# Performance work log

Measured on AMD Instinct MI355X. Metric: run time of the kernel, lower is better.

## Reference

```python
import jax, jax.numpy as jnp
import numpy as np

B, S, D_IN = 4, 2048, 1024
H, D_HEAD = 16, 64  # per-head output dim d_output=64


def setup_inputs() -> dict:
    key = jax.random.key(0)
    ks = jax.random.split(key, 9)
    s_in = 1.0 / np.sqrt(D_IN)
    s_o = 1.0 / np.sqrt(H * D_HEAD)
    return {
        "x": jax.random.normal(ks[0], (B, S, D_IN), dtype=jnp.float32),
        "Wq": jax.random.uniform(ks[1], (H, D_IN, D_HEAD), jnp.float32, -s_in, s_in),
        "bq": jax.random.uniform(ks[2], (H, D_HEAD), jnp.float32, -s_in, s_in),
        "Wk": jax.random.uniform(ks[3], (H, D_IN, D_HEAD), jnp.float32, -s_in, s_in),
        "bk": jax.random.uniform(ks[4], (H, D_HEAD), jnp.float32, -s_in, s_in),
        "Wv": jax.random.uniform(ks[5], (H, D_IN, D_HEAD), jnp.float32, -s_in, s_in),
        "bv": jax.random.uniform(ks[6], (H, D_HEAD), jnp.float32, -s_in, s_in),
        "Wo": jax.random.uniform(ks[7], (H * D_HEAD, D_HEAD), jnp.float32, -s_o, s_o),
        "bo": jax.random.uniform(ks[8], (D_HEAD,), jnp.float32, -s_o, s_o),
    }


def reference(x, Wq, bq, Wk, bk, Wv, bv, Wo, bo):
    # per-head projections: [B,H,S,Dh]
    q = jnp.einsum("bsd,hde->bhse", x, Wq) + bq[None, :, None, :]
    k = jnp.einsum("bsd,hde->bhse", x, Wk) + bk[None, :, None, :]
    v = jnp.einsum("bsd,hde->bhse", x, Wv) + bv[None, :, None, :]
    scale = 1.0 / np.sqrt(D_HEAD)
    scores = jnp.einsum("bhqe,bhke->bhqk", q, k) * scale  # [B,H,S,S]
    seq_len = x.shape[1]
    causal = jnp.tril(jnp.ones((seq_len, seq_len), dtype=bool))
    scores = jnp.where(causal[None, None], scores, -jnp.inf)
    attn = jax.nn.softmax(scores, axis=-1)  # dropout=0 -> identity
    out = jnp.einsum("bhqk,bhke->bhqe", attn, v)  # [B,H,S,Dh]
    # concat heads along feature dim (head order matches torch cat)
    out = out.transpose(0, 2, 1, 3).reshape(x.shape[0], seq_len, H * D_HEAD)
    return out @ Wo + bo
```

## Files before the change

kernel.cpp:

```cpp
#include <hip/hip_runtime.h>

typedef unsigned short u16;
typedef unsigned int u32;
typedef __attribute__((ext_vector_type(8))) short s16x8;
typedef __attribute__((ext_vector_type(4))) float f32x4;

#define MFMA(a,b,c) __builtin_amdgcn_mfma_f32_16x16x32_bf16((a),(b),(c),0,0,0)
#define QSCALE 0.18033688011112042f

__device__ __forceinline__ u16 bfc(float f){
  union { float f; unsigned int u; } c; c.f = f;
  return (u16)((c.u + 0x7fffu + ((c.u >> 16) & 1u)) >> 16);
}
__device__ __forceinline__ u32 pkbf(float lo, float hi){
  union { float f; u32 u; } a, b; a.f = lo; b.f = hi;
  return __builtin_amdgcn_perm(b.u + 0x8000u, a.u + 0x8000u, 0x07060302u);
}
__device__ __forceinline__ float fexp2(float x){ return __builtin_amdgcn_exp2f(x); }
__device__ __forceinline__ f32x4 zero4(){ f32x4 z; z[0]=0.f; z[1]=0.f; z[2]=0.f; z[3]=0.f; return z; }

__device__ __forceinline__ void gload_lds16(const u16* g, u16* l){
  __builtin_amdgcn_global_load_lds((const __attribute__((address_space(1))) unsigned int*)g,
                                   (__attribute__((address_space(3))) unsigned int*)l, 16, 0, 0);
}

__global__ __launch_bounds__(256) void k_cvt(const float* __restrict__ x, u16* __restrict__ xb){
  int i = (blockIdx.x * 256 + threadIdx.x) * 4;
  float4 v = *(const float4*)(x + i);
  *(uint2*)(xb + i) = make_uint2(pkbf(v.x, v.y), pkbf(v.z, v.w));
}

__global__ __launch_bounds__(256) void k_twp(const float* __restrict__ Wq, const float* __restrict__ Wk,
    const float* __restrict__ Wv, const float* __restrict__ Wo,
    u16* __restrict__ wt, u16* __restrict__ wot){
  __shared__ float t[64][65];
  int y = blockIdx.y, k0 = blockIdx.x * 64, tid = threadIdx.x;
  const float* src; u16* dst;
  if (y < 16)      { src = Wq + (size_t)y * 65536;        dst = wt + (size_t)y * 65536; }
  else if (y < 32) { src = Wk + (size_t)(y-16) * 65536;   dst = wt + (size_t)y * 65536; }
  else if (y < 48) { src = Wv + (size_t)(y-32) * 65536;   dst = wt + (size_t)y * 65536; }
  else             { src = Wo;                            dst = wot; }
  const float* s = src + (size_t)k0 * 64;
  int kl = tid >> 2, nc = (tid & 3) * 16;
  #pragma unroll
  for (int j = 0; j < 4; j++){
    float4 v = *(const float4*)(s + kl * 64 + nc + j * 4);
    t[kl][nc + j*4 + 0] = v.x; t[kl][nc + j*4 + 1] = v.y;
    t[kl][nc + j*4 + 2] = v.z; t[kl][nc + j*4 + 3] = v.w;
  }
  __syncthreads();
  int n = tid >> 2, kc = (tid & 3) * 16;
  u16 o[16];
  #pragma unroll
  for (int j = 0; j < 16; j++) o[j] = bfc(t[kc + j][n]);
  u16* d = dst + (size_t)n * 1024 + k0 + kc;
  *(uint4*)(d)     = *(uint4*)&o[0];
  *(uint4*)(d + 8) = *(uint4*)&o[8];
}

__global__ __launch_bounds__(256) void k_qkv(const u16* __restrict__ xb, const u16* __restrict__ wt,
    const float* __restrict__ bq, const float* __restrict__ bk, const float* __restrict__ bv,
    u16* __restrict__ Qo, u16* __restrict__ Ko, u16* __restrict__ VT){
  __shared__ u16 As[128][64];
  __shared__ u16 Bs[128][64];
  int tid = threadIdx.x, wave = tid >> 6, lane = tid & 63;
  int l16 = lane & 15, g = lane >> 4;
  int row0 = blockIdx.x * 128, col0 = blockIdx.y * 128;
  int wm = (wave & 1) * 64, wn = (wave >> 1) * 64;
  f32x4 acc[4][4];
  #pragma unroll
  for (int mt = 0; mt < 4; mt++)
    #pragma unroll
    for (int nt = 0; nt < 4; nt++) acc[mt][nt] = zero4();
  int srow = (lane >> 3);
  int scol = ((lane & 7) ^ srow) * 8;
  for (int k0 = 0; k0 < 1024; k0 += 64){
    __syncthreads();
    #pragma unroll
    for (int p = 0; p < 4; p++){
      int r = wave * 32 + p * 8 + srow;
      gload_lds16(xb + (size_t)(row0 + r) * 1024 + k0 + scol, &As[wave * 32 + p * 8][0]);
      gload_lds16(wt + (size_t)(col0 + r) * 1024 + k0 + scol, &Bs[wave * 32 + p * 8][0]);
    }
    __syncthreads();
    #pragma unroll
    for (int c = 0; c < 2; c++){
      s16x8 af[4], bf[4];
      #pragma unroll
      for (int mt = 0; mt < 4; mt++)
        af[mt] = *(const s16x8*)&As[wm + mt*16 + l16][((c*4 + g) ^ (l16 & 7)) * 8];
      #pragma unroll
      for (int nt = 0; nt < 4; nt++)
        bf[nt] = *(const s16x8*)&Bs[wn + nt*16 + l16][((c*4 + g) ^ (l16 & 7)) * 8];
      #pragma unroll
      for (int mt = 0; mt < 4; mt++)
        #pragma unroll
        for (int nt = 0; nt < 4; nt++) acc[mt][nt] = MFMA(af[mt], bf[nt], acc[mt][nt]);
    }
  }
  #pragma unroll
  for (int nt = 0; nt < 4; nt++){
    int n = col0 + wn + nt * 16 + l16;
    int wi = n >> 10, hh = (n >> 6) & 15, dh = n & 63;
    const float* bptr = (wi == 0) ? bq : (wi == 1) ? bk : bv;
    float bval = bptr[hh * 64 + dh];
    #pragma unroll
    for (int mt = 0; mt < 4; mt++){
      int m0 = row0 + wm + mt * 16 + g * 4;
      int bb = m0 >> 11, ss = m0 & 2047;
      if (wi == 2){
        u32 p0 = pkbf(acc[mt][nt][0] + bval, acc[mt][nt][1] + bval);
        u32 p1 = pkbf(acc[mt][nt][2] + bval, acc[mt][nt][3] + bval);
        *(uint2*)&VT[(((size_t)bb * 16 + hh) * 64 + dh) * 2048 + ss] = make_uint2(p0, p1);
      } else {
        u16* dst = (wi == 0) ? Qo : Ko;
        float scl = (wi == 0) ? QSCALE : 1.0f;
        #pragma unroll
        for (int i = 0; i < 4; i++)
          dst[(((size_t)bb * 16 + hh) * 2048 + ss + i) * 64 + dh] = bfc((acc[mt][nt][i] + bval) * scl);
      }
    }
  }
}

__global__ __launch_bounds__(256, 2) void k_attn(const u16* __restrict__ Q, const u16* __restrict__ Kg,
    const u16* __restrict__ VT, u16* __restrict__ O){
  __shared__ u16 smem[18432];
  u16* Ks = smem;
  u16* Vt = smem + 4608;
  u16* Ps = smem + 9216;
  float* mg = (float*)smem;
  float* lg = (float*)smem + 8192;
  int hbi = blockIdx.x, pair = blockIdx.y;
  int b = hbi >> 4, h = hbi & 15;
  int tid = threadIdx.x, wave = tid >> 6, lane = tid & 63;
  int l16 = lane & 15, g = lane >> 4;
  int qg = wave >> 1, kg = wave & 1;
  size_t hb = (size_t)hbi * 2048 * 64;
  const u16* kbase = Kg + hb;
  const u16* vbase = VT + hb;
  int sr = tid >> 3, scc = (tid & 7) * 8;
  u16* PsW = Ps + wave * (4 * 16 * 36);
  #pragma unroll
  for (int ph = 0; ph < 2; ph++){
    int qt = ph ? pair : (15 - pair);
    int qbase = qt * 128;
    int q0 = qbase + qg * 64;
    s16x8 bq[4][2];
    #pragma unroll
    for (int j = 0; j < 4; j++)
      #pragma unroll
      for (int c = 0; c < 2; c++)
        bq[j][c] = *(const s16x8*)(Q + hb + (size_t)(q0 + j*16 + l16) * 64 + c*32 + g*8);
    f32x4 accO[4][4];
    #pragma unroll
    for (int mt = 0; mt < 4; mt++)
      #pragma unroll
      for (int j = 0; j < 4; j++) accO[mt][j] = zero4();
    f32x4 rsacc = zero4();
    int nkt = 2 * qt + 2;
    uint4 ka0, ka1, va0, va1;
    __syncthreads();
    ka0 = *(const uint4*)(kbase + (size_t)(sr)      * 64 + scc);
    ka1 = *(const uint4*)(kbase + (size_t)(sr + 32) * 64 + scc);
    va0 = *(const uint4*)(vbase + (size_t)(sr)      * 2048 + scc);
    va1 = *(const uint4*)(vbase + (size_t)(sr + 32) * 2048 + scc);
    *(uint4*)&Ks[sr * 72 + scc] = ka0; *(uint4*)&Ks[(sr + 32) * 72 + scc] = ka1;
    *(uint4*)&Vt[sr * 72 + scc] = va0; *(uint4*)&Vt[(sr + 32) * 72 + scc] = va1;
    __syncthreads();
    for (int kt = 0; kt < nkt; kt++){
      if (kt + 1 < nkt){
        int kb2 = (kt + 1) * 64;
        ka0 = *(const uint4*)(kbase + (size_t)(kb2 + sr)      * 64 + scc);
        ka1 = *(const uint4*)(kbase + (size_t)(kb2 + sr + 32) * 64 + scc);
        va0 = *(const uint4*)(vbase + (size_t)(sr)      * 2048 + kb2 + scc);
        va1 = *(const uint4*)(vbase + (size_t)(sr + 32) * 2048 + kb2 + scc);
      }
      int ks0 = kt * 64 + kg * 32;
      if (ks0 <= q0 + 63){
        s16x8 ak[2][2], av[4];
        #pragma unroll
        for (int t = 0; t < 2; t++)
          #pragma unroll
          for (int c = 0; c < 2; c++)
            ak[t][c] = *(const s16x8*)&Ks[(kg*32 + t*16 + l16) * 72 + c*32 + g*8];
        #pragma unroll
        for (int mt = 0; mt < 4; mt++)
          av[mt] = *(const s16x8*)&Vt[(mt*16 + l16) * 72 + kg*32 + g*8];
        #pragma unroll
        for (int j = 0; j < 4; j++){
          f32x4 s0 = zero4(), s1 = zero4();
          s0 = MFMA(ak[0][0], bq[j][0], s0);
          s0 = MFMA(ak[0][1], bq[j][1], s0);
          s1 = MFMA(ak[1][0], bq[j][0], s1);
          s1 = MFMA(ak[1][1], bq[j][1], s1);
          if (ks0 + 31 > q0 + j*16){
            int qrow = q0 + j*16 + l16;
            #pragma unroll
            for (int r = 0; r < 4; r++){
              if (ks0 + g*4 + r      > qrow) s0[r] = -1e30f;
              if (ks0 + 16 + g*4 + r > qrow) s1[r] = -1e30f;
            }
          }
          float p00 = fexp2(s0[0]), p01 = fexp2(s0[1]), p02 = fexp2(s0[2]), p03 = fexp2(s0[3]);
          float p10 = fexp2(s1[0]), p11 = fexp2(s1[1]), p12 = fexp2(s1[2]), p13 = fexp2(s1[3]);
          rsacc[j] += ((p00 + p01) + (p02 + p03)) + ((p10 + p11) + (p12 + p13));
          u16* pr = PsW + (j*16 + l16) * 36;
          *(uint2*)&pr[g*4]      = make_uint2(pkbf(p00, p01), pkbf(p02, p03));
          *(uint2*)&pr[16 + g*4] = make_uint2(pkbf(p10, p11), pkbf(p12, p13));
        }
        #pragma unroll
        for (int j = 0; j < 4; j++){
          s16x8 bp = *(const s16x8*)&PsW[(j*16 + l16) * 36 + g*8];
          #pragma unroll
          for (int mt = 0; mt < 4; mt++)
            accO[mt][j] = MFMA(av[mt], bp, accO[mt][j]);
        }
      }
      if (kt + 1 < nkt){
        __syncthreads();
        *(uint4*)&Ks[sr * 72 + scc] = ka0; *(uint4*)&Ks[(sr + 32) * 72 + scc] = ka1;
        *(uint4*)&Vt[sr * 72 + scc] = va0; *(uint4*)&Vt[(sr + 32) * 72 + scc] = va1;
        __syncthreads();
      }
    }
    __syncthreads();
    if (kg == 1){
      #pragma unroll
      for (int mt = 0; mt < 4; mt++)
        #pragma unroll
        for (int j = 0; j < 4; j++)
          *(f32x4*)&mg[((qg*16 + mt*4 + j) * 64 + lane) * 4] = accO[mt][j];
      *(f32x4*)&lg[(qg*64 + lane) * 4] = rsacc;
    }
    __syncthreads();
    if (kg == 0){
      f32x4 lpart = *(f32x4*)&lg[(qg*64 + lane) * 4];
      float rinv[4];
      #pragma unroll
      for (int j = 0; j < 4; j++){
        float l = rsacc[j] + lpart[j];
        l += __shfl_xor(l, 16);
        l += __shfl_xor(l, 32);
        rinv[j] = 1.0f / l;
      }
      #pragma unroll
      for (int mt = 0; mt < 4; mt++)
        #pragma unroll
        for (int j = 0; j < 4; j++){
          f32x4 part = *(f32x4*)&mg[((qg*16 + mt*4 + j) * 64 + lane) * 4];
          float o0 = (accO[mt][j][0] + part[0]) * rinv[j];
          float o1 = (accO[mt][j][1] + part[1]) * rinv[j];
          float o2 = (accO[mt][j][2] + part[2]) * rinv[j];
          float o3 = (accO[mt][j][3] + part[3]) * rinv[j];
          *(uint2*)&O[((size_t)b * 2048 + q0 + j*16 + l16) * 1024 + h*64 + mt*16 + g*4] =
              make_uint2(pkbf(o0, o1), pkbf(o2, o3));
        }
    }
  }
}

__global__ __launch_bounds__(256) void k_oproj(const u16* __restrict__ Ob, const u16* __restrict__ wot,
    const float* __restrict__ bo, float* __restrict__ out){
  __shared__ u16 As[64][72];
  __shared__ u16 Bs[64][72];
  int rb = blockIdx.x, kc = blockIdx.y;
  int tid = threadIdx.x, wave = tid >> 6, lane = tid & 63;
  int l16 = lane & 15, g = lane >> 4;
  int wr = (wave & 1) * 32, wc = (wave >> 1) * 32;
  int row0 = rb * 64;
  f32x4 acc[2][2];
  acc[0][0]=zero4(); acc[0][1]=zero4(); acc[1][0]=zero4(); acc[1][1]=zero4();
  int r0s = tid >> 3, cc0 = (tid & 7) * 8, r1s = r0s + 32;
  for (int k0 = kc * 256; k0 < kc * 256 + 256; k0 += 64){
    __syncthreads();
    *(uint4*)&As[r0s][cc0] = *(const uint4*)(Ob + (size_t)(row0 + r0s) * 1024 + k0 + cc0);
    *(uint4*)&As[r1s][cc0] = *(const uint4*)(Ob + (size_t)(row0 + r1s) * 1024 + k0 + cc0);
    *(uint4*)&Bs[r0s][cc0] = *(const uint4*)(wot + (size_t)r0s * 1024 + k0 + cc0);
    *(uint4*)&Bs[r1s][cc0] = *(const uint4*)(wot + (size_t)r1s * 1024 + k0 + cc0);
    __syncthreads();
    #pragma unroll
    for (int c = 0; c < 2; c++){
      int kcc = c * 32;
      s16x8 a0 = *(const s16x8*)&As[wr      + l16][kcc + g * 8];
      s16x8 a1 = *(const s16x8*)&As[wr + 16 + l16][kcc + g * 8];
      s16x8 b0 = *(const s16x8*)&Bs[wc      + l16][kcc + g * 8];
      s16x8 b1 = *(const s16x8*)&Bs[wc + 16 + l16][kcc + g * 8];
      acc[0][0] = MFMA(a0, b0, acc[0][0]);
      acc[0][1] = MFMA(a0, b1, acc[0][1]);
      acc[1][0] = MFMA(a1, b0, acc[1][0]);
      acc[1][1] = MFMA(a1, b1, acc[1][1]);
    }
  }
  #pragma unroll
  for (int rt = 0; rt < 2; rt++){
    #pragma unroll
    for (int ct = 0; ct < 2; ct++){
      int col = wc + ct * 16 + l16;
      float bval = (kc == 0) ? bo[col] : 0.f;
      #pragma unroll
      for (int i = 0; i < 4; i++){
        int row = row0 + wr + rt * 16 + g * 4 + i;
        atomicAdd(&out[(size_t)row * 64 + col], acc[rt][ct][i] + bval);
      }
    }
  }
}

extern "C" void kernel_launch(void* const* d_in, const int* in_sizes, int n_in,
                              void* d_out, int out_size, void* d_ws, size_t ws_size,
                              hipStream_t stream){
  const float* x  = (const float*)d_in[0];
  const float* Wq = (const float*)d_in[1];
  const float* bq = (const float*)d_in[2];
  const float* Wk = (const float*)d_in[3];
  const float* bk = (const float*)d_in[4];
  const float* Wv = (const float*)d_in[5];
  const float* bv = (const float*)d_in[6];
  const float* Wo = (const float*)d_in[7];
  const float* bo = (const float*)d_in[8];

  u16* xb  = (u16*)d_ws;
  u16* wt  = xb  + 8388608;
  u16* wot = wt  + 3145728;
  u16* Qb  = wot + 65536;
  u16* Kb  = Qb  + 8388608;
  u16* VTb = Kb  + 8388608;
  u16* Ob  = xb;
  float* out = (float*)d_out;

  hipMemsetAsync(d_out, 0, (size_t)out_size * sizeof(float), stream);
  k_cvt<<<8192, 256, 0, stream>>>(x, xb);
  k_twp<<<dim3(16, 49), 256, 0, stream>>>(Wq, Wk, Wv, Wo, wt, wot);
  k_qkv<<<dim3(64, 24), 256, 0, stream>>>(xb, wt, bq, bk, bv, Qb, Kb, VTb);
  k_attn<<<dim3(64, 8), 256, 0, stream>>>(Qb, Kb, VTb, Ob);
  k_oproj<<<dim3(128, 4), 256, 0, stream>>>(Ob, wot, bo, out);
}
```

Before: 244.9 us.

## Drop shared K/V staging in attention and split work across 8 waves

The attention kernel stops staging K and V tiles through shared memory with block-wide barriers. Each wave now loads its K and V fragments straight from global memory (relying on cache) and skips fully masked tiles independently. The block grows to 512 threads, with each wave owning 32 query rows instead of 64, which halves per-wave accumulators and should raise occupancy. The trade-off is that K/V data is read redundantly by several waves from global/L2 instead of being shared in LDS.

Measured after the change: 299.5 us. 1.22x slower.

```diff
diff --git a/kernel.cpp b/kernel.cpp
--- a/kernel.cpp
+++ b/kernel.cpp
@@ -123,12 +123,9 @@
   }
 }
 
-__global__ __launch_bounds__(256, 2) void k_attn(const u16* __restrict__ Q, const u16* __restrict__ Kg,
+__global__ __launch_bounds__(512, 4) void k_attn(const u16* __restrict__ Q, const u16* __restrict__ Kg,
     const u16* __restrict__ VT, u16* __restrict__ O){
-  __shared__ u16 smem[18432];
-  u16* Ks = smem;
-  u16* Vt = smem + 4608;
-  u16* Ps = smem + 9216;
+  __shared__ u16 smem[17408];
   float* mg = (float*)smem;
   float* lg = (float*)smem + 8192;
   int hbi = blockIdx.x, pair = blockIdx.y;
@@ -139,89 +136,67 @@
   size_t hb = (size_t)hbi * 2048 * 64;
   const u16* kbase = Kg + hb;
   const u16* vbase = VT + hb;
-  int sr = tid >> 3, scc = (tid & 7) * 8;
-  u16* PsW = Ps + wave * (4 * 16 * 36);
+  u16* PsW = smem + wave * 1152;
+  const u16* vrow[4];
+  #pragma unroll
+  for (int mt = 0; mt < 4; mt++) vrow[mt] = vbase + (size_t)(mt*16 + l16) * 2048 + g*8;
   #pragma unroll
   for (int ph = 0; ph < 2; ph++){
     int qt = ph ? pair : (15 - pair);
     int qbase = qt * 128;
-    int q0 = qbase + qg * 64;
-    s16x8 bq[4][2];
-    #pragma unroll
-    for (int j = 0; j < 4; j++)
+    int q0 = qbase + qg * 32;
+    s16x8 bq[2][2];
+    #pragma unroll
+    for (int j = 0; j < 2; j++)
       #pragma unroll
       for (int c = 0; c < 2; c++)
         bq[j][c] = *(const s16x8*)(Q + hb + (size_t)(q0 + j*16 + l16) * 64 + c*32 + g*8);
-    f32x4 accO[4][4];
-    #pragma unroll
-    for (int mt = 0; mt < 4; mt++)
-      #pragma unroll
-      for (int j = 0; j < 4; j++) accO[mt][j] = zero4();
-    f32x4 rsacc = zero4();
+    f32x4 accO[4][2];
+    #pragma unroll
+    for (int mt = 0; mt < 4; mt++){ accO[mt][0] = zero4(); accO[mt][1] = zero4(); }
+    float rsacc[2] = {0.f, 0.f};
     int nkt = 2 * qt + 2;
-    uint4 ka0, ka1, va0, va1;
-    __syncthreads();
-    ka0 = *(const uint4*)(kbase + (size_t)(sr)      * 64 + scc);
-    ka1 = *(const uint4*)(kbase + (size_t)(sr + 32) * 64 + scc);
-    va0 = *(const uint4*)(vbase + (size_t)(sr)      * 2048 + scc);
-    va1 = *(const uint4*)(vbase + (size_t)(sr + 32) * 2048 + scc);
-    *(uint4*)&Ks[sr * 72 + scc] = ka0; *(uint4*)&Ks[(sr + 32) * 72 + scc] = ka1;
-    *(uint4*)&Vt[sr * 72 + scc] = va0; *(uint4*)&Vt[(sr + 32) * 72 + scc] = va1;
     __syncthreads();
     for (int kt = 0; kt < nkt; kt++){
-      if (kt + 1 < nkt){
-        int kb2 = (kt + 1) * 64;
-        ka0 = *(const uint4*)(kbase + (size_t)(kb2 + sr)      * 64 + scc);
-        ka1 = *(const uint4*)(kbase + (size_t)(kb2 + sr + 32) * 64 + scc);
-        va0 = *(const uint4*)(vbase + (size_t)(sr)      * 2048 + kb2 + scc);
-        va1 = *(const uint4*)(vbase + (size_t)(sr + 32) * 2048 + kb2 + scc);
-      }
       int ks0 = kt * 64 + kg * 32;
-      if (ks0 <= q0 + 63){
-        s16x8 ak[2][2], av[4];
-        #pragma unroll
-        for (int t = 0; t < 2; t++)
+      if (ks0 > q0 + 31) continue;
+      s16x8 ak[2][2], av[4];
+      #pragma unroll
+      for (int t = 0; t < 2; t++)
+        #pragma unroll
+        for (int c = 0; c < 2; c++)
+          ak[t][c] = *(const s16x8*)(kbase + (size_t)(ks0 + t*16 + l16) * 64 + c*32 + g*8);
+      #pragma unroll
+      for (int mt = 0; mt < 4; mt++)
+        av[mt] = *(const s16x8*)(vrow[mt] + ks0);
+      #pragma unroll
+      for (int j = 0; j < 2; j++){
+        f32x4 s0 = zero4(), s1 = zero4();
+        s0 = MFMA(ak[0][0], bq[j][0], s0);
+        s0 = MFMA(ak[0][1], bq[j][1], s0);
+        s1 = MFMA(ak[1][0], bq[j][0], s1);
+        s1 = MFMA(ak[1][1], bq[j][1], s1);
+        if (ks0 + 31 > q0 + j*16){
+          int qrow = q0 + j*16 + l16;
           #pragma unroll
-          for (int c = 0; c < 2; c++)
-            ak[t][c] = *(const s16x8*)&Ks[(kg*32 + t*16 + l16) * 72 + c*32 + g*8];
+          for (int r = 0; r < 4; r++){
+            if (ks0 + g*4 + r      > qrow) s0[r] = -1e30f;
+            if (ks0 + 16 + g*4 + r > qrow) s1[r] = -1e30f;
+          }
+        }
+        float p00 = fexp2(s0[0]), p01 = fexp2(s0[1]), p02 = fexp2(s0[2]), p03 = fexp2(s0[3]);
+        float p10 = fexp2(s1[0]), p11 = fexp2(s1[1]), p12 = fexp2(s1[2]), p13 = fexp2(s1[3]);
+        rsacc[j] += ((p00 + p01) + (p02 + p03)) + ((p10 + p11) + (p12 + p13));
+        u16* pr = PsW + (j*16 + l16) * 36;
+        *(uint2*)&pr[g*4]      = make_uint2(pkbf(p00, p01), pkbf(p02, p03));
+        *(uint2*)&pr[16 + g*4] = make_uint2(pkbf(p10, p11), pkbf(p12, p13));
+      }
+      #pragma unroll
+      for (int j = 0; j < 2; j++){
+        s16x8 bp = *(const s16x8*)&PsW[(j*16 + l16) * 36 + g*8];
         #pragma unroll
         for (int mt = 0; mt < 4; mt++)
-          av[mt] = *(const s16x8*)&Vt[(mt*16 + l16) * 72 + kg*32 + g*8];
-        #pragma unroll
-        for (int j = 0; j < 4; j++){
-          f32x4 s0 = zero4(), s1 = zero4();
-          s0 = MFMA(ak[0][0], bq[j][0], s0);
-          s0 = MFMA(ak[0][1], bq[j][1], s0);
-          s1 = MFMA(ak[1][0], bq[j][0], s1);
-          s1 = MFMA(ak[1][1], bq[j][1], s1);
-          if (ks0 + 31 > q0 + j*16){
-            int qrow = q0 + j*16 + l16;
-            #pragma unroll
-            for (int r = 0; r < 4; r++){
-              if (ks0 + g*4 + r      > qrow) s0[r] = -1e30f;
-              if (ks0 + 16 + g*4 + r > qrow) s1[r] = -1e30f;
-            }
-          }
-          float p00 = fexp2(s0[0]), p01 = fexp2(s0[1]), p02 = fexp2(s0[2]), p03 = fexp2(s0[3]);
-          float p10 = fexp2(s1[0]), p11 = fexp2(s1[1]), p12 = fexp2(s1[2]), p13 = fexp2(s1[3]);
-          rsacc[j] += ((p00 + p01) + (p02 + p03)) + ((p10 + p11) + (p12 + p13));
-          u16* pr = PsW + (j*16 + l16) * 36;
-          *(uint2*)&pr[g*4]      = make_uint2(pkbf(p00, p01), pkbf(p02, p03));
-          *(uint2*)&pr[16 + g*4] = make_uint2(pkbf(p10, p11), pkbf(p12, p13));
-        }
-        #pragma unroll
-        for (int j = 0; j < 4; j++){
-          s16x8 bp = *(const s16x8*)&PsW[(j*16 + l16) * 36 + g*8];
-          #pragma unroll
-          for (int mt = 0; mt < 4; mt++)
-            accO[mt][j] = MFMA(av[mt], bp, accO[mt][j]);
-        }
-      }
-      if (kt + 1 < nkt){
-        __syncthreads();
-        *(uint4*)&Ks[sr * 72 + scc] = ka0; *(uint4*)&Ks[(sr + 32) * 72 + scc] = ka1;
-        *(uint4*)&Vt[sr * 72 + scc] = va0; *(uint4*)&Vt[(sr + 32) * 72 + scc] = va1;
-        __syncthreads();
+          accO[mt][j] = MFMA(av[mt], bp, accO[mt][j]);
       }
     }
     __syncthreads();
@@ -229,17 +204,17 @@
       #pragma unroll
       for (int mt = 0; mt < 4; mt++)
         #pragma unroll
-        for (int j = 0; j < 4; j++)
-          *(f32x4*)&mg[((qg*16 + mt*4 + j) * 64 + lane) * 4] = accO[mt][j];
-      *(f32x4*)&lg[(qg*64 + lane) * 4] = rsacc;
+        for (int j = 0; j < 2; j++)
+          *(f32x4*)&mg[((qg*8 + mt*2 + j) * 64 + lane) * 4] = accO[mt][j];
+      lg[(qg*64 + lane)*2 + 0] = rsacc[0];
+      lg[(qg*64 + lane)*2 + 1] = rsacc[1];
     }
     __syncthreads();
     if (kg == 0){
-      f32x4 lpart = *(f32x4*)&lg[(qg*64 + lane) * 4];
-      float rinv[4];
-      #pragma unroll
-      for (int j = 0; j < 4; j++){
-        float l = rsacc[j] + lpart[j];
+      float rinv[2];
+      #pragma unroll
+      for (int j = 0; j < 2; j++){
+        float l = rsacc[j] + lg[(qg*64 + lane)*2 + j];
         l += __shfl_xor(l, 16);
         l += __shfl_xor(l, 32);
         rinv[j] = 1.0f / l;
@@ -247,8 +222,8 @@
       #pragma unroll
       for (int mt = 0; mt < 4; mt++)
         #pragma unroll
-        for (int j = 0; j < 4; j++){
-          f32x4 part = *(f32x4*)&mg[((qg*16 + mt*4 + j) * 64 + lane) * 4];
+        for (int j = 0; j < 2; j++){
+          f32x4 part = *(f32x4*)&mg[((qg*8 + mt*2 + j) * 64 + lane) * 4];
           float o0 = (accO[mt][j][0] + part[0]) * rinv[j];
           float o1 = (accO[mt][j][1] + part[1]) * rinv[j];
           float o2 = (accO[mt][j][2] + part[2]) * rinv[j];
@@ -333,6 +308,6 @@
   k_cvt<<<8192, 256, 0, stream>>>(x, xb);
   k_twp<<<dim3(16, 49), 256, 0, stream>>>(Wq, Wk, Wv, Wo, wt, wot);
   k_qkv<<<dim3(64, 24), 256, 0, stream>>>(xb, wt, bq, bk, bv, Qb, Kb, VTb);
-  k_attn<<<dim3(64, 8), 256, 0, stream>>>(Qb, Kb, VTb, Ob);
+  k_attn<<<dim3(64, 8), 512, 0, stream>>>(Qb, Kb, VTb, Ob);
   k_oproj<<<dim3(128, 4), 256, 0, stream>>>(Ob, wot, bo, out);
 }
```

## Merge conversion kernels and stage 128-key K/V tiles per barrier in attention

Applied to the files above, without the earlier changes.

Merges the x conversion and weight transpose kernels into one launch, with a flat block index deciding which job each block does. The attention kernel now loads 128 keys of K and V per stage instead of 64 and processes them as two 64-key substeps. This halves the number of barrier pairs and global-to-LDS staging rounds. The cost is more LDS (about 54KB) and more staging registers, which may limit occupancy at two blocks per CU.

Result: slower. 292.0 us (+19.2%).

```diff
diff --git a/kernel.cpp b/kernel.cpp
--- a/kernel.cpp
+++ b/kernel.cpp
@@ -24,17 +24,20 @@
                                    (__attribute__((address_space(3))) unsigned int*)l, 16, 0, 0);
 }
 
-__global__ __launch_bounds__(256) void k_cvt(const float* __restrict__ x, u16* __restrict__ xb){
-  int i = (blockIdx.x * 256 + threadIdx.x) * 4;
-  float4 v = *(const float4*)(x + i);
-  *(uint2*)(xb + i) = make_uint2(pkbf(v.x, v.y), pkbf(v.z, v.w));
-}
-
-__global__ __launch_bounds__(256) void k_twp(const float* __restrict__ Wq, const float* __restrict__ Wk,
+__global__ __launch_bounds__(256) void k_prep(const float* __restrict__ x, u16* __restrict__ xb,
+    const float* __restrict__ Wq, const float* __restrict__ Wk,
     const float* __restrict__ Wv, const float* __restrict__ Wo,
     u16* __restrict__ wt, u16* __restrict__ wot){
   __shared__ float t[64][65];
-  int y = blockIdx.y, k0 = blockIdx.x * 64, tid = threadIdx.x;
+  int bid = blockIdx.x, tid = threadIdx.x;
+  if (bid < 8192){
+    int i = (bid * 256 + tid) * 4;
+    float4 v = *(const float4*)(x + i);
+    *(uint2*)(xb + i) = make_uint2(pkbf(v.x, v.y), pkbf(v.z, v.w));
+    return;
+  }
+  int tt = bid - 8192;
+  int y = tt >> 4, k0 = (tt & 15) * 64;
   const float* src; u16* dst;
   if (y < 16)      { src = Wq + (size_t)y * 65536;        dst = wt + (size_t)y * 65536; }
   else if (y < 32) { src = Wk + (size_t)(y-16) * 65536;   dst = wt + (size_t)y * 65536; }
@@ -125,10 +128,10 @@
 
 __global__ __launch_bounds__(256, 2) void k_attn(const u16* __restrict__ Q, const u16* __restrict__ Kg,
     const u16* __restrict__ VT, u16* __restrict__ O){
-  __shared__ u16 smem[18432];
+  __shared__ u16 smem[27136];
   u16* Ks = smem;
-  u16* Vt = smem + 4608;
-  u16* Ps = smem + 9216;
+  u16* Vt = smem + 9216;
+  u16* Ps = smem + 17920;
   float* mg = (float*)smem;
   float* lg = (float*)smem + 8192;
   int hbi = blockIdx.x, pair = blockIdx.y;
@@ -140,7 +143,8 @@
   const u16* kbase = Kg + hb;
   const u16* vbase = VT + hb;
   int sr = tid >> 3, scc = (tid & 7) * 8;
-  u16* PsW = Ps + wave * (4 * 16 * 36);
+  int vr = tid >> 4, vcc = (tid & 15) * 8;
+  u16* PsW = Ps + wave * 2304;
   #pragma unroll
   for (int ph = 0; ph < 2; ph++){
     int qt = ph ? pair : (15 - pair);
@@ -158,69 +162,81 @@
       #pragma unroll
       for (int j = 0; j < 4; j++) accO[mt][j] = zero4();
     f32x4 rsacc = zero4();
-    int nkt = 2 * qt + 2;
-    uint4 ka0, ka1, va0, va1;
-    __syncthreads();
-    ka0 = *(const uint4*)(kbase + (size_t)(sr)      * 64 + scc);
-    ka1 = *(const uint4*)(kbase + (size_t)(sr + 32) * 64 + scc);
-    va0 = *(const uint4*)(vbase + (size_t)(sr)      * 2048 + scc);
-    va1 = *(const uint4*)(vbase + (size_t)(sr + 32) * 2048 + scc);
-    *(uint4*)&Ks[sr * 72 + scc] = ka0; *(uint4*)&Ks[(sr + 32) * 72 + scc] = ka1;
-    *(uint4*)&Vt[sr * 72 + scc] = va0; *(uint4*)&Vt[(sr + 32) * 72 + scc] = va1;
-    __syncthreads();
-    for (int kt = 0; kt < nkt; kt++){
-      if (kt + 1 < nkt){
-        int kb2 = (kt + 1) * 64;
-        ka0 = *(const uint4*)(kbase + (size_t)(kb2 + sr)      * 64 + scc);
-        ka1 = *(const uint4*)(kbase + (size_t)(kb2 + sr + 32) * 64 + scc);
-        va0 = *(const uint4*)(vbase + (size_t)(sr)      * 2048 + kb2 + scc);
-        va1 = *(const uint4*)(vbase + (size_t)(sr + 32) * 2048 + kb2 + scc);
-      }
-      int ks0 = kt * 64 + kg * 32;
-      if (ks0 <= q0 + 63){
-        s16x8 ak[2][2], av[4];
-        #pragma unroll
-        for (int t = 0; t < 2; t++)
+    int nst = qt + 1;
+    uint4 ka[4], va[4];
+    __syncthreads();
+    #pragma unroll
+    for (int m = 0; m < 4; m++){
+      ka[m] = *(const uint4*)(kbase + (size_t)(sr + 32*m) * 64 + scc);
+      va[m] = *(const uint4*)(vbase + (size_t)(vr + 16*m) * 2048 + vcc);
+    }
+    #pragma unroll
+    for (int m = 0; m < 4; m++){
+      *(uint4*)&Ks[(sr + 32*m) * 72 + scc] = ka[m];
+      *(uint4*)&Vt[(vr + 16*m) * 136 + vcc] = va[m];
+    }
+    __syncthreads();
+    for (int st = 0; st < nst; st++){
+      if (st + 1 < nst){
+        int kb2 = (st + 1) * 128;
+        #pragma unroll
+        for (int m = 0; m < 4; m++){
+          ka[m] = *(const uint4*)(kbase + (size_t)(kb2 + sr + 32*m) * 64 + scc);
+          va[m] = *(const uint4*)(vbase + (size_t)(vr + 16*m) * 2048 + kb2 + vcc);
+        }
+      }
+      #pragma unroll
+      for (int s = 0; s < 2; s++){
+        int kl = s * 64 + kg * 32;
+        int ks0 = st * 128 + kl;
+        if (ks0 <= q0 + 63){
+          s16x8 ak[2][2], av[4];
           #pragma unroll
-          for (int c = 0; c < 2; c++)
-            ak[t][c] = *(const s16x8*)&Ks[(kg*32 + t*16 + l16) * 72 + c*32 + g*8];
-        #pragma unroll
-        for (int mt = 0; mt < 4; mt++)
-          av[mt] = *(const s16x8*)&Vt[(mt*16 + l16) * 72 + kg*32 + g*8];
-        #pragma unroll
-        for (int j = 0; j < 4; j++){
-          f32x4 s0 = zero4(), s1 = zero4();
-          s0 = MFMA(ak[0][0], bq[j][0], s0);
-          s0 = MFMA(ak[0][1], bq[j][1], s0);
-          s1 = MFMA(ak[1][0], bq[j][0], s1);
-          s1 = MFMA(ak[1][1], bq[j][1], s1);
-          if (ks0 + 31 > q0 + j*16){
-            int qrow = q0 + j*16 + l16;
+          for (int t = 0; t < 2; t++)
             #pragma unroll
-            for (int r = 0; r < 4; r++){
-              if (ks0 + g*4 + r      > qrow) s0[r] = -1e30f;
-              if (ks0 + 16 + g*4 + r > qrow) s1[r] = -1e30f;
-            }
-          }
-          float p00 = fexp2(s0[0]), p01 = fexp2(s0[1]), p02 = fexp2(s0[2]), p03 = fexp2(s0[3]);
-          float p10 = fexp2(s1[0]), p11 = fexp2(s1[1]), p12 = fexp2(s1[2]), p13 = fexp2(s1[3]);
-          rsacc[j] += ((p00 + p01) + (p02 + p03)) + ((p10 + p11) + (p12 + p13));
-          u16* pr = PsW + (j*16 + l16) * 36;
-          *(uint2*)&pr[g*4]      = make_uint2(pkbf(p00, p01), pkbf(p02, p03));
-          *(uint2*)&pr[16 + g*4] = make_uint2(pkbf(p10, p11), pkbf(p12, p13));
-        }
-        #pragma unroll
-        for (int j = 0; j < 4; j++){
-          s16x8 bp = *(const s16x8*)&PsW[(j*16 + l16) * 36 + g*8];
+            for (int c = 0; c < 2; c++)
+              ak[t][c] = *(const s16x8*)&Ks[(kl + t*16 + l16) * 72 + c*32 + g*8];
           #pragma unroll
           for (int mt = 0; mt < 4; mt++)
-            accO[mt][j] = MFMA(av[mt], bp, accO[mt][j]);
+            av[mt] = *(const s16x8*)&Vt[(mt*16 + l16) * 136 + kl + g*8];
+          #pragma unroll
+          for (int j = 0; j < 4; j++){
+            f32x4 s0 = zero4(), s1 = zero4();
+            s0 = MFMA(ak[0][0], bq[j][0], s0);
+            s0 = MFMA(ak[0][1], bq[j][1], s0);
+            s1 = MFMA(ak[1][0], bq[j][0], s1);
+            s1 = MFMA(ak[1][1], bq[j][1], s1);
+            if (ks0 + 31 > q0 + j*16){
+              int qrow = q0 + j*16 + l16;
+              #pragma unroll
+              for (int r = 0; r < 4; r++){
+                if (ks0 + g*4 + r      > qrow) s0[r] = -1e30f;
+                if (ks0 + 16 + g*4 + r > qrow) s1[r] = -1e30f;
+              }
+            }
+            float p00 = fexp2(s0[0]), p01 = fexp2(s0[1]), p02 = fexp2(s0[2]), p03 = fexp2(s0[3]);
+            float p10 = fexp2(s1[0]), p11 = fexp2(s1[1]), p12 = fexp2(s1[2]), p13 = fexp2(s1[3]);
+            rsacc[j] += ((p00 + p01) + (p02 + p03)) + ((p10 + p11) + (p12 + p13));
+            u16* pr = PsW + (j*16 + l16) * 36;
+            *(uint2*)&pr[g*4]      = make_uint2(pkbf(p00, p01), pkbf(p02, p03));
+            *(uint2*)&pr[16 + g*4] = make_uint2(pkbf(p10, p11), pkbf(p12, p13));
+          }
+          #pragma unroll
+          for (int j = 0; j < 4; j++){
+            s16x8 bp = *(const s16x8*)&PsW[(j*16 + l16) * 36 + g*8];
+            #pragma unroll
+            for (int mt = 0; mt < 4; mt++)
+              accO[mt][j] = MFMA(av[mt], bp, accO[mt][j]);
+          }
         }
       }
-      if (kt + 1 < nkt){
+      if (st + 1 < nst){
         __syncthreads();
-        *(uint4*)&Ks[sr * 72 + scc] = ka0; *(uint4*)&Ks[(sr + 32) * 72 + scc] = ka1;
-        *(uint4*)&Vt[sr * 72 + scc] = va0; *(uint4*)&Vt[(sr + 32) * 72 + scc] = va1;
+        #pragma unroll
+        for (int m = 0; m < 4; m++){
+          *(uint4*)&Ks[(sr + 32*m) * 72 + scc] = ka[m];
+          *(uint4*)&Vt[(vr + 16*m) * 136 + vcc] = va[m];
+        }
         __syncthreads();
       }
     }
@@ -330,8 +346,7 @@
   float* out = (float*)d_out;
 
   hipMemsetAsync(d_out, 0, (size_t)out_size * sizeof(float), stream);
-  k_cvt<<<8192, 256, 0, stream>>>(x, xb);
-  k_twp<<<dim3(16, 49), 256, 0, stream>>>(Wq, Wk, Wv, Wo, wt, wot);
+  k_prep<<<8976, 256, 0, stream>>>(x, xb, Wq, Wk, Wv, Wo, wt, wot);
   k_qkv<<<dim3(64, 24), 256, 0, stream>>>(xb, wt, bq, bk, bv, Qb, Kb, VTb);
   k_attn<<<dim3(64, 8), 256, 0, stream>>>(Qb, Kb, VTb, Ob);
   k_oproj<<<dim3(128, 4), 256, 0, stream>>>(Ob, wot, bo, out);
```
